# Optimization experiments

Hardware: AMD Instinct MI355X
Metric: run time of the kernel (lower is better)

The kernel has to match this reference:

```python
import jax, jax.numpy as jnp
import numpy as np

L = 4096   # num_tokens (one prefill sequence)
D = 2048   # hidden_size
HK = 16    # num_k_heads
HV = 32    # num_v_heads
DK = 128   # head_k_dim
DV = 128   # head_v_dim
RATIO = HV // HK
EPS = 1e-6


def setup_inputs() -> dict:
    key = jax.random.key(0)
    ks = jax.random.split(key, 11)
    s = 0.02
    return {
        "hidden_states": jax.random.normal(ks[0], (L, D), jnp.float32),
        "Wq": jax.random.normal(ks[1], (D, HK * DK), jnp.float32) * s,
        "Wk": jax.random.normal(ks[2], (D, HK * DK), jnp.float32) * s,
        "Wv": jax.random.normal(ks[3], (D, HV * DV), jnp.float32) * s,
        "Wz": jax.random.normal(ks[4], (D, HV * DV), jnp.float32) * s,
        "Wb": jax.random.normal(ks[5], (D, HV), jnp.float32) * s,
        "Wa": jax.random.normal(ks[6], (D, HV), jnp.float32) * s,
        "A_log": jnp.log(jax.random.uniform(ks[7], (HV,), jnp.float32, 1.0, 16.0)),
        "dt_bias": jax.random.normal(ks[8], (HV,), jnp.float32) * 0.5,
        "norm_weight": jnp.ones((DV,), jnp.float32),
        "W_out": jax.random.normal(ks[9], (HV * DV, D), jnp.float32) * s,
    }


def _l2norm(x):
    return x * jax.lax.rsqrt(jnp.sum(x * x, axis=-1, keepdims=True) + EPS)


def reference(hidden_states, Wq, Wk, Wv, Wz, Wb, Wa, A_log, dt_bias, norm_weight, W_out):
    h = hidden_states
    # --- input projections (qkvz + ba split) ---
    q = _l2norm((h @ Wq).reshape(L, HK, DK))            # [L, HK, DK]
    k = _l2norm((h @ Wk).reshape(L, HK, DK))
    v = (h @ Wv).reshape(L, HV, DV)                     # [L, HV, DV]
    z = (h @ Wz).reshape(L, HV, DV)                     # gate for RMSNorm
    beta = jax.nn.sigmoid(h @ Wb)                       # [L, HV]
    g = -jnp.exp(A_log) * jax.nn.softplus(h @ Wa + dt_bias)  # [L, HV]
    decay = jnp.exp(g)                                  # per-token per-head decay
    # repeat shared q/k heads to value heads (GQA ratio)
    q = jnp.repeat(q, RATIO, axis=1) * (DK ** -0.5)     # [L, HV, DK]
    k = jnp.repeat(k, RATIO, axis=1)

    # --- gated delta rule recurrence over tokens ---
    def step(S, xs):
        q_t, k_t, v_t, b_t, d_t = xs                    # [HV,DK],[HV,DK],[HV,DV],[HV],[HV]
        S = S * d_t[:, None, None]                      # decay state [HV, DK, DV]
        pred = jnp.einsum('hk,hkv->hv', k_t, S)         # memory readout
        delta = (v_t - pred) * b_t[:, None]             # delta-rule correction
        S = S + k_t[:, :, None] * delta[:, None, :]
        o = jnp.einsum('hk,hkv->hv', q_t, S)
        return S, o

    S0 = jnp.zeros((HV, DK, DV), jnp.float32)
    _, core = jax.lax.scan(step, S0, (q, k, v, beta, decay))  # core: [L, HV, DV]

    # --- gated RMSNorm: x * silu(z), rms-normalize over head dim ---
    x = core * jax.nn.silu(z)
    x = x * jax.lax.rsqrt(jnp.mean(x * x, axis=-1, keepdims=True) + EPS) * norm_weight

    # --- output projection ---
    return x.reshape(L, HV * DV) @ W_out                # [L, D]
```

## Files before the change

kernel.cpp:

```cpp
#include <hip/hip_runtime.h>

#define LTOK 4096
#define DHID 2048
#define HKN  16
#define HVN  32
#define DKK  128
#define NTOT 12288

typedef unsigned short u16;
typedef __attribute__((ext_vector_type(8))) short short8;
typedef __attribute__((ext_vector_type(8))) unsigned short u16x8;
typedef __attribute__((ext_vector_type(4))) unsigned short u16x4;
typedef __attribute__((ext_vector_type(4))) float f32x4;

__device__ __forceinline__ float b2f(u16 u) {
  unsigned int x = ((unsigned int)u) << 16;
  return __builtin_bit_cast(float, x);
}
__device__ __forceinline__ u16 f2bf(float f) {
  unsigned int u = __builtin_bit_cast(unsigned int, f);
  u += 0x7FFFu + ((u >> 16) & 1u);
  return (u16)(u >> 16);
}

template<int C> __device__ __forceinline__ float dppmv(float x) {
  int i = __builtin_amdgcn_update_dpp(0, __builtin_bit_cast(int, x), C, 0xF, 0xF, true);
  return __builtin_bit_cast(float, i);
}
__device__ __forceinline__ float red16(float x) {
  x += dppmv<0xB1>(x);
  x += dppmv<0x4E>(x);
  x += dppmv<0x124>(x);
  x += dppmv<0x128>(x);
  return x;
}

__device__ __forceinline__ void gld16(const void* g, void* l) {
  __builtin_amdgcn_global_load_lds((const __attribute__((address_space(1))) void*)g,
                                   (__attribute__((address_space(3))) void*)l, 16, 0, 0);
}

__device__ __forceinline__ int sw16(int r, int c, int rowc) { return (r * rowc + c) ^ ((r & 7) << 3); }

__device__ __forceinline__ void cstore(u16* C, size_t i, float v) { C[i] = f2bf(v); }
__device__ __forceinline__ void cstore(float* C, size_t i, float v) { C[i] = v; }

__global__ __launch_bounds__(256)
void k_cvt(const float* __restrict__ s, u16* __restrict__ d, int n) {
  const int i = (blockIdx.x * 256 + threadIdx.x) * 4;
  const float4 v = *(const float4*)(s + i);
  ushort4 o;
  o.x = f2bf(v.x); o.y = f2bf(v.y); o.z = f2bf(v.z); o.w = f2bf(v.w);
  *(ushort4*)(d + i) = o;
}

__global__ __launch_bounds__(256)
void k_tr(const float* __restrict__ src, u16* __restrict__ dst, int R, int C) {
  __shared__ float tl[32][33];
  const int r0 = blockIdx.y * 32, c0 = blockIdx.x * 32;
  const int tr = threadIdx.x >> 3, tc = (threadIdx.x & 7) * 4;
  const float4 v = *(const float4*)(src + (size_t)(r0 + tr) * C + c0 + tc);
  tl[tr][tc] = v.x; tl[tr][tc + 1] = v.y; tl[tr][tc + 2] = v.z; tl[tr][tc + 3] = v.w;
  __syncthreads();
  ushort4 o;
  o.x = f2bf(tl[tc + 0][tr]); o.y = f2bf(tl[tc + 1][tr]);
  o.z = f2bf(tl[tc + 2][tr]); o.w = f2bf(tl[tc + 3][tr]);
  *(ushort4*)(dst + (size_t)(c0 + tr) * R + r0 + tc) = o;
}

#define MFMA16(a, b, c) __builtin_amdgcn_mfma_f32_16x16x32_bf16(a, b, c, 0, 0, 0)

template<typename OutT>
__global__ __launch_bounds__(512, 2)
void k_g256(const u16* __restrict__ A, const u16* __restrict__ Bt, OutT* __restrict__ C,
            int M, int N, int K, int NT) {
  __shared__ u16 Lds[4][16384];
  const int tid = threadIdx.x;
  const int lane = tid & 63, w = tid >> 6;
  const int fr = lane & 15, fq = lane >> 4;
  const int wm = (w >> 2) * 128, wn = (w & 3) * 64;
  const int nkt = K >> 5;
  const size_t sK = (size_t)K;

  const int MT = gridDim.x / NT;
  const int nts = (NT < 16) ? NT : 16;
  const int per_super = MT * nts;
  const int super = blockIdx.x / per_super;
  const int within = blockIdx.x % per_super;
  const int mtg = MT >> 3;
  const int q = within >> 3;
  const int mt = (within & 7) * mtg + (q % mtg);
  const int nt = super * nts + q / mtg;

  const int kslot = ((tid & 3) ^ ((tid >> 3) & 3)) * 8;
  const u16* aS = A + (size_t)(mt * 256 + (tid >> 2)) * sK + kslot;
  const u16* bS = Bt + (size_t)(nt * 256 + (tid >> 2)) * sK + kslot;

  f32x4 acc[8][4] = {};

#define STAGE(kt_) {                                                          \
    const int sk = ((kt_) < nkt) ? (kt_) : (nkt - 1);                         \
    u16* La = &Lds[(kt_) & 3][w * 512];                                       \
    u16* Lb = &Lds[(kt_) & 3][8192 + w * 512];                                \
    gld16(aS + (size_t)sk * 32, La);                                          \
    gld16(aS + 128 * sK + (size_t)sk * 32, La + 4096);                        \
    gld16(bS + (size_t)sk * 32, Lb);                                          \
    gld16(bS + 128 * sK + (size_t)sk * 32, Lb + 4096); }

  STAGE(0)
  STAGE(1)
  STAGE(2)

  const int akey = (fr >> 1) & 3;
  for (int kt = 0; kt < nkt; ++kt) {
    STAGE(kt + 3)
    asm volatile("s_waitcnt vmcnt(12)" ::: "memory");
    __builtin_amdgcn_s_barrier();
    const u16* Lc = Lds[kt & 3];
    short8 af[8], bf[4];
#pragma unroll
    for (int i = 0; i < 8; ++i)
      af[i] = *(const short8*)&Lc[(wm + i * 16 + fr) * 32 + ((fq ^ akey) << 3)];
#pragma unroll
    for (int j = 0; j < 4; ++j)
      bf[j] = *(const short8*)&Lc[8192 + (wn + j * 16 + fr) * 32 + ((fq ^ akey) << 3)];
    asm volatile("s_waitcnt lgkmcnt(0)" ::: "memory");
    __builtin_amdgcn_s_barrier();
    __builtin_amdgcn_s_setprio(1);
#pragma unroll
    for (int i = 0; i < 8; ++i)
#pragma unroll
      for (int j = 0; j < 4; ++j)
        acc[i][j] = MFMA16(af[i], bf[j], acc[i][j]);
    __builtin_amdgcn_s_setprio(0);
  }
#undef STAGE

  const int r0 = mt * 256 + wm + fq * 4;
  const int c0 = nt * 256 + wn + fr;
#pragma unroll
  for (int i = 0; i < 8; ++i)
#pragma unroll
    for (int j = 0; j < 4; ++j)
#pragma unroll
      for (int e = 0; e < 4; ++e)
        cstore(C, (size_t)(r0 + i * 16 + e) * N + c0 + j * 16, acc[i][j][e]);
}

__global__ __launch_bounds__(256)
void k_ba(const float* __restrict__ h, const float* __restrict__ Wb, const float* __restrict__ Wa,
          const float* __restrict__ A_log, const float* __restrict__ dtb,
          float* __restrict__ beta, float* __restrict__ g_out) {
  const int w = threadIdx.x >> 6, lane = threadIdx.x & 63;
  const int t = blockIdx.x * 4 + w;
  const int j = lane & 31;
  const bool isB = lane < 32;
  const float* __restrict__ hr = h + (size_t)t * DHID;
  const float* Wc = isB ? Wb : Wa;
  float acc = 0.f;
  for (int kk = 0; kk < DHID; ++kk) acc = fmaf(hr[kk], Wc[(size_t)kk * HVN + j], acc);
  if (isB) {
    beta[(size_t)t * HVN + j] = 1.f / (1.f + expf(-acc));
  } else {
    float xx = acc + dtb[j];
    float sp = (xx > 20.f) ? xx : log1pf(expf(xx));
    g_out[(size_t)t * HVN + j] = -expf(A_log[j]) * sp;
  }
}

__global__ __launch_bounds__(256)
void k_l2n(u16* __restrict__ qkvz) {
  const int w = threadIdx.x >> 6, lane = threadIdx.x & 63;
  const int r = blockIdx.x * 4 + w;
  const int isK = r >> 16;
  const int rr = r & 65535;
  const int t = rr >> 4, hd = rr & 15;
  u16* p = qkvz + (size_t)t * NTOT + isK * 2048 + hd * DKK + lane * 2;
  float a = b2f(p[0]), b = b2f(p[1]);
  float ss = a * a + b * b;
  ss = red16(ss);
  ss += __shfl_xor(ss, 16);
  ss += __shfl_xor(ss, 32);
  const float sc = rsqrtf(ss + 1e-6f) * (isK ? 1.f : 0.08838834764831845f);
  p[0] = f2bf(a * sc); p[1] = f2bf(b * sc);
}

__global__ __launch_bounds__(256)
void k_r1(const u16* __restrict__ qkvz, const float* __restrict__ beta_g,
          const float* __restrict__ g_g, u16* __restrict__ UM_g, float* __restrict__ cumL_g) {
  const int pair = blockIdx.x;
  const int hv = pair >> 6, n = pair & 63;
  const int hk = hv >> 1;
  const int t0 = n * 64;
  const int tid = threadIdx.x, lane = tid & 63, wv = tid >> 6;
  const int fr = lane & 15, fq = lane >> 4;

  __shared__ __align__(16) u16 Xb[256 * 64];
  __shared__ __align__(16) u16 Dbuf0[64 * 64 * 2];
  __shared__ __align__(16) u16 Dbuf1[64 * 64 * 2];
  __shared__ float Lc[64];
  __shared__ float Bc[64];
  u16* Kl = Dbuf0;

  const int j = tid & 63, h = tid >> 6;
  const u16* kg = qkvz + (size_t)(t0 + j) * NTOT + 2048 + hk * DKK + h * 32;
  const u16* vg = qkvz + (size_t)(t0 + j) * NTOT + 4096 + hv * DKK + h * 32;
  u16x8 kv[4], vv[4];
#pragma unroll
  for (int i = 0; i < 4; ++i) { kv[i] = *(const u16x8*)(kg + i * 8); vv[i] = *(const u16x8*)(vg + i * 8); }
  if (tid < 64) {
    Lc[tid] = g_g[(size_t)(t0 + tid) * HVN + hv];
    Bc[tid] = beta_g[(size_t)(t0 + tid) * HVN + hv];
  }
#pragma unroll
  for (int i = 0; i < 4; ++i) *(u16x8*)&Kl[sw16(j, h * 32 + i * 8, 128)] = kv[i];
  __syncthreads();
  if (tid == 0) { float a = 0.f; for (int t = 0; t < 64; ++t) { a += Lc[t]; Lc[t] = a; } }
  __syncthreads();
  if (tid < 64) cumL_g[(size_t)pair * 64 + tid] = Lc[tid];

  {
    const float bj = Bc[j];
    const float mj = bj * __expf(Lc[j]);
#pragma unroll
    for (int i = 0; i < 4; ++i)
#pragma unroll
      for (int e = 0; e < 8; ++e) {
        int c = h * 32 + i * 8 + e;
        Xb[sw16(c, j, 64)] = f2bf(bj * b2f(vv[i][e]));
        Xb[sw16(128 + c, j, 64)] = f2bf(mj * b2f(kv[i][e]));
      }
  }
  f32x4 kk[4] = {};
#pragma unroll
  for (int ks = 0; ks < 4; ++ks) {
    short8 afr = *(const short8*)&Kl[sw16(wv * 16 + fr, ks * 32 + fq * 8, 128)];
#pragma unroll
    for (int ct = 0; ct < 4; ++ct) {
      short8 bfr = *(const short8*)&Kl[sw16(ct * 16 + fr, ks * 32 + fq * 8, 128)];
      kk[ct] = MFMA16(afr, bfr, kk[ct]);
    }
  }
  __syncthreads();

  f32x4 acc[16];
#pragma unroll
  for (int ct = 0; ct < 16; ++ct) {
    u16x4 xi = *(const u16x4*)&Xb[sw16(ct * 16 + fr, wv * 16 + fq * 4, 64)];
    acc[ct][0] = b2f(xi[0]); acc[ct][1] = b2f(xi[1]); acc[ct][2] = b2f(xi[2]); acc[ct][3] = b2f(xi[3]);
  }
#pragma unroll
  for (int ct = 0; ct < 4; ++ct) {
    const int s = ct * 16 + fr;
    u16x4 pk;
#pragma unroll
    for (int e = 0; e < 4; ++e) {
      const int t = wv * 16 + fq * 4 + e;
      float v = (s < t) ? -Bc[t] * __expf(Lc[t] - Lc[s]) * kk[ct][e] : 0.f;
      pk[e] = f2bf(v);
      Dbuf0[sw16(t, s, 64)] = pk[e];
    }
    *(u16x4*)&Dbuf0[4096 + sw16(s, wv * 16 + fq * 4, 64)] = pk;
  }
  __syncthreads();

  u16* DA = Dbuf0;
  u16* DB = Dbuf1;
  for (int stg = 0; stg < 6; ++stg) {
    u16* Dr = DA;
    u16* Dc = DA + 4096;
    short8 da0 = *(const short8*)&Dr[sw16(wv * 16 + fr, 0 + fq * 8, 64)];
    short8 da1 = *(const short8*)&Dr[sw16(wv * 16 + fr, 32 + fq * 8, 64)];
#pragma unroll
    for (int ct = 0; ct < 16; ++ct) {
      short8 b0 = *(const short8*)&Xb[sw16(ct * 16 + fr, 0 + fq * 8, 64)];
      short8 b1 = *(const short8*)&Xb[sw16(ct * 16 + fr, 32 + fq * 8, 64)];
      acc[ct] = MFMA16(da0, b0, acc[ct]);
      acc[ct] = MFMA16(da1, b1, acc[ct]);
    }
    f32x4 sq[4] = {};
    if (stg < 5) {
#pragma unroll
      for (int ct = 0; ct < 4; ++ct) {
        short8 sb0 = *(const short8*)&Dc[sw16(ct * 16 + fr, 0 + fq * 8, 64)];
        short8 sb1 = *(const short8*)&Dc[sw16(ct * 16 + fr, 32 + fq * 8, 64)];
        sq[ct] = MFMA16(da0, sb0, sq[ct]);
        sq[ct] = MFMA16(da1, sb1, sq[ct]);
      }
    }
    __syncthreads();
#pragma unroll
    for (int ct = 0; ct < 16; ++ct) {
      u16x4 pk;
      pk[0] = f2bf(acc[ct][0]); pk[1] = f2bf(acc[ct][1]); pk[2] = f2bf(acc[ct][2]); pk[3] = f2bf(acc[ct][3]);
      *(u16x4*)&Xb[sw16(ct * 16 + fr, wv * 16 + fq * 4, 64)] = pk;
    }
    if (stg < 5) {
#pragma unroll
      for (int ct = 0; ct < 4; ++ct) {
        u16x4 pk;
        pk[0] = f2bf(sq[ct][0]); pk[1] = f2bf(sq[ct][1]); pk[2] = f2bf(sq[ct][2]); pk[3] = f2bf(sq[ct][3]);
        *(u16x4*)&(DB + 4096)[sw16(ct * 16 + fr, wv * 16 + fq * 4, 64)] = pk;
#pragma unroll
        for (int e = 0; e < 4; ++e) DB[sw16(wv * 16 + fq * 4 + e, ct * 16 + fr, 64)] = pk[e];
      }
    }
    __syncthreads();
    u16* tmp = DA; DA = DB; DB = tmp;
  }

#pragma unroll
  for (int ct = 0; ct < 16; ++ct) {
    const int c = ct * 16 + fr;
#pragma unroll
    for (int e = 0; e < 4; ++e) {
      const int t = wv * 16 + fq * 4 + e;
      float v = acc[ct][e];
      if (ct >= 8) v = -v;
      UM_g[((size_t)pair * 64 + t) * 256 + c] = f2bf(v);
    }
  }
}

__global__ __launch_bounds__(512)
void k_r2(u16* __restrict__ qkvz, const u16* __restrict__ UM_g,
          const float* __restrict__ cumL_g, u16* __restrict__ o1_g) {
  const int hv = blockIdx.x >> 1, cs = blockIdx.x & 1;
  const int hk = hv >> 1;
  const int tid = threadIdx.x, lane = tid & 63, w = tid >> 6;
  const int fr = lane & 15, fq = lane >> 4;
  const int j = tid & 63, h = tid >> 6;

  __shared__ __align__(16) u16 Ml2[2][8192];
  __shared__ __align__(16) u16 Ql2[2][8192];
  __shared__ __align__(16) u16 Kt2[2][8192];
  __shared__ __align__(16) u16 Ul2[2][4096];
  __shared__ __align__(16) u16 dT[4096];
  __shared__ __align__(16) u16 SbT[8192];
  __shared__ __align__(16) u16 o1b[4096];
  __shared__ float Lc2[2][64];

  const int tw = w & 3;
  const int d0 = (w >> 2) * 2;

  f32x4 sacc[4];
#pragma unroll
  for (int d = 0; d < 4; ++d) sacc[d] = (f32x4){0.f, 0.f, 0.f, 0.f};
  for (int i = tid; i < 8192; i += 512) SbT[i] = 0;

  u16x8 pQ0, pQ1, pK0, pK1, pM0, pM1, pU0;
  float pL, pL63;

#define PREF(nn) {                                                            \
    const int nc = ((nn) < 64) ? (nn) : 63;                                   \
    const int pr = hv * 64 + nc; const int tt0 = nc * 64;                     \
    const u16* qg = qkvz + (size_t)(tt0 + j) * NTOT + hk * DKK + h * 16;      \
    pQ0 = *(const u16x8*)qg;          pQ1 = *(const u16x8*)(qg + 8);          \
    pK0 = *(const u16x8*)(qg + 2048); pK1 = *(const u16x8*)(qg + 2056);       \
    const u16* mg = UM_g + ((size_t)pr * 64 + j) * 256;                       \
    pM0 = *(const u16x8*)(mg + 128 + h * 16);                                 \
    pM1 = *(const u16x8*)(mg + 136 + h * 16);                                 \
    pU0 = *(const u16x8*)(mg + cs * 64 + h * 8);                              \
    pL = cumL_g[(size_t)pr * 64 + j]; pL63 = cumL_g[(size_t)pr * 64 + 63]; }

#define STW(b) {                                                              \
    *(u16x8*)&Ql2[b][sw16(j, h * 16, 128)] = pQ0;                             \
    *(u16x8*)&Ql2[b][sw16(j, h * 16 + 8, 128)] = pQ1;                         \
    *(u16x8*)&Ml2[b][sw16(j, h * 16, 128)] = pM0;                             \
    *(u16x8*)&Ml2[b][sw16(j, h * 16 + 8, 128)] = pM1;                         \
    const float scK = __expf(pL63 - pL);                                      \
    _Pragma("unroll")                                                         \
    for (int e = 0; e < 8; ++e) {                                             \
      Kt2[b][sw16(h * 16 + e, j, 64)] = f2bf(scK * b2f(pK0[e]));              \
      Kt2[b][sw16(h * 16 + 8 + e, j, 64)] = f2bf(scK * b2f(pK1[e]));          \
      Ul2[b][sw16(h * 8 + e, j, 64)] = pU0[e];                                \
    }                                                                         \
    if (h == 0) Lc2[b][j] = pL; }

  PREF(0)
  STW(0)
  __syncthreads();

  for (int n = 0; n < 64; ++n) {
    const int cur = n & 1;
    const int pair = hv * 64 + n, t0 = n * 64;
    const float curL63 = pL63;
    PREF(n + 1)

    short8 amf[4], aqf[4];
#pragma unroll
    for (int ks = 0; ks < 4; ++ks) {
      amf[ks] = *(const short8*)&Ml2[cur][sw16(tw * 16 + fr, ks * 32 + fq * 8, 128)];
      aqf[ks] = *(const short8*)&Ql2[cur][sw16(tw * 16 + fr, ks * 32 + fq * 8, 128)];
    }
    float el[4];
#pragma unroll
    for (int e = 0; e < 4; ++e) el[e] = __expf(Lc2[cur][tw * 16 + fq * 4 + e]);
#pragma unroll
    for (int dd = 0; dd < 2; ++dd) {
      const int d = d0 + dd;
      u16x4 uv = *(const u16x4*)&Ul2[cur][sw16(d * 16 + fr, tw * 16 + fq * 4, 64)];
      f32x4 dc;
      dc[0] = b2f(uv[0]); dc[1] = b2f(uv[1]); dc[2] = b2f(uv[2]); dc[3] = b2f(uv[3]);
      f32x4 oc = {};
#pragma unroll
      for (int ks = 0; ks < 4; ++ks) {
        short8 bs = *(const short8*)&SbT[sw16(d * 16 + fr, ks * 32 + fq * 8, 128)];
        dc = MFMA16(amf[ks], bs, dc);
        oc = MFMA16(aqf[ks], bs, oc);
      }
      u16x4 pk;
      pk[0] = f2bf(dc[0]); pk[1] = f2bf(dc[1]); pk[2] = f2bf(dc[2]); pk[3] = f2bf(dc[3]);
      *(u16x4*)&dT[sw16(d * 16 + fr, tw * 16 + fq * 4, 64)] = pk;
#pragma unroll
      for (int e = 0; e < 4; ++e)
        o1b[sw16(tw * 16 + fq * 4 + e, d * 16 + fr, 64)] = f2bf(oc[e] * el[e]);
    }
    __syncthreads();

    {
      const int i = tid * 8;
      u16x8 vd = *(const u16x8*)&dT[i];
      const int f = cs * 4096 + i;
      *(u16x8*)(qkvz + (size_t)(t0 + (f >> 7)) * NTOT + 4096 + hv * DKK + (f & 127)) = vd;
      u16x8 vo = *(const u16x8*)&o1b[i];
      *(u16x8*)(o1_g + (size_t)pair * 8192 + (size_t)(i >> 6) * 128 + cs * 64 + (i & 63)) = vo;
    }
    STW(cur ^ 1)
    {
      const float eC = __expf(curL63);
      short8 ak0 = *(const short8*)&Kt2[cur][sw16(w * 16 + fr, fq * 8, 64)];
      short8 ak1 = *(const short8*)&Kt2[cur][sw16(w * 16 + fr, 32 + fq * 8, 64)];
#pragma unroll
      for (int d = 0; d < 4; ++d) {
        short8 bd0 = *(const short8*)&dT[sw16(d * 16 + fr, fq * 8, 64)];
        short8 bd1 = *(const short8*)&dT[sw16(d * 16 + fr, 32 + fq * 8, 64)];
        f32x4 sa = sacc[d];
#pragma unroll
        for (int e = 0; e < 4; ++e) sa[e] *= eC;
        sa = MFMA16(ak0, bd0, sa);
        sa = MFMA16(ak1, bd1, sa);
        sacc[d] = sa;
        u16x4 pk;
        pk[0] = f2bf(sa[0]); pk[1] = f2bf(sa[1]); pk[2] = f2bf(sa[2]); pk[3] = f2bf(sa[3]);
        *(u16x4*)&SbT[sw16(d * 16 + fr, w * 16 + fq * 4, 128)] = pk;
      }
    }
    __syncthreads();
  }
#undef PREF
#undef STW
}

__global__ __launch_bounds__(512)
void k_r3(const u16* __restrict__ qkvz, const u16* __restrict__ o1_g,
          const float* __restrict__ cumL_g, const float* __restrict__ nw,
          u16* __restrict__ x) {
  const int pair = blockIdx.x, hv = pair >> 6, n = pair & 63, hk = hv >> 1, t0 = n * 64;
  const int tid = threadIdx.x, lane = tid & 63, w = tid >> 6;
  const int fr = lane & 15, fq = lane >> 4;
  const int j = tid & 63, h = tid >> 6;

  __shared__ __align__(16) u16 Ql[8192];
  __shared__ __align__(16) u16 Kl[8192];
  __shared__ __align__(16) u16 Gl[4096];
  __shared__ __align__(16) u16 dTl[8192];
  __shared__ __align__(16) float of[64 * 132];
  __shared__ float Lc[64];
  __shared__ float Lw[128];

  {
    const u16* qg = qkvz + (size_t)(t0 + j) * NTOT + hk * DKK + h * 16;
    u16x8 q0 = *(const u16x8*)qg, q1 = *(const u16x8*)(qg + 8);
    u16x8 k0 = *(const u16x8*)(qg + 2048), k1 = *(const u16x8*)(qg + 2056);
    *(u16x8*)&Ql[sw16(j, h * 16, 128)] = q0;
    *(u16x8*)&Ql[sw16(j, h * 16 + 8, 128)] = q1;
    *(u16x8*)&Kl[sw16(j, h * 16, 128)] = k0;
    *(u16x8*)&Kl[sw16(j, h * 16 + 8, 128)] = k1;
  }
#pragma unroll
  for (int it = 0; it < 2; ++it) {
    const int f = ((w * 2 + it) * 64 + lane) * 8;
    gld16(qkvz + (size_t)(t0 + (f >> 7)) * NTOT + 4096 + hv * DKK + (f & 127),
          (char*)dTl + (w * 2 + it) * 1024);
  }
  if (tid < 64) Lc[tid] = cumL_g[(size_t)pair * 64 + tid];
  if (tid < 128) Lw[tid] = nw[tid];
  __syncthreads();

  const int tw = w & 3, sp = (w >> 2) * 2;
  {
    f32x4 kk0 = {}, kk1 = {};
#pragma unroll
    for (int ks = 0; ks < 4; ++ks) {
      short8 aq = *(const short8*)&Ql[sw16(tw * 16 + fr, ks * 32 + fq * 8, 128)];
      short8 b0 = *(const short8*)&Kl[sw16(sp * 16 + fr, ks * 32 + fq * 8, 128)];
      short8 b1 = *(const short8*)&Kl[sw16((sp + 1) * 16 + fr, ks * 32 + fq * 8, 128)];
      kk0 = MFMA16(aq, b0, kk0);
      kk1 = MFMA16(aq, b1, kk1);
    }
#pragma unroll
    for (int e = 0; e < 4; ++e) {
      const int t = tw * 16 + fq * 4 + e;
      const float Lt = Lc[t];
      const int s0 = sp * 16 + fr, s1 = s0 + 16;
      Gl[sw16(t, s0, 64)] = f2bf((s0 <= t) ? kk0[e] * __expf(Lt - Lc[s0]) : 0.f);
      Gl[sw16(t, s1, 64)] = f2bf((s1 <= t) ? kk1[e] * __expf(Lt - Lc[s1]) : 0.f);
    }
  }
  __syncthreads();

  {
    short8 ag0 = *(const short8*)&Gl[sw16(tw * 16 + fr, fq * 8, 64)];
    short8 ag1 = *(const short8*)&Gl[sw16(tw * 16 + fr, 32 + fq * 8, 64)];
#pragma unroll
    for (int dd = 0; dd < 4; ++dd) {
      const int d = (w >> 2) * 4 + dd;
      short8 bd0 = *(const short8*)&dTl[sw16(d * 16 + fr, fq * 8, 64)];
      short8 bd1 = *(const short8*)&dTl[sw16(d * 16 + fr, 32 + fq * 8, 64)];
      f32x4 oc = {};
      oc = MFMA16(ag0, bd0, oc);
      oc = MFMA16(ag1, bd1, oc);
#pragma unroll
      for (int e = 0; e < 4; ++e) of[(tw * 16 + fq * 4 + e) * 132 + d * 16 + fr] = oc[e];
    }
  }
  __syncthreads();

  {
    const int t = tid >> 3, q8 = tid & 7;
    const u16* zp = qkvz + (size_t)(t0 + t) * NTOT + 8192 + hv * DKK + q8 * 16;
    const u16* op = o1_g + (size_t)pair * 8192 + t * 128;
    float xv[16];
    float ss = 0.f;
#pragma unroll
    for (int i = 0; i < 2; ++i) {
      u16x8 zv = *(const u16x8*)(zp + i * 8);
      u16x8 ov = *(const u16x8*)(op + (((q8 * 16 + i * 8) ^ ((t & 7) << 3))));
#pragma unroll
      for (int e = 0; e < 8; ++e) {
        float z = b2f(zv[e]);
        float o = of[t * 132 + q8 * 16 + i * 8 + e] + b2f(ov[e]);
        float xx = o * (z / (1.f + __expf(-z)));
        xv[i * 8 + e] = xx;
        ss = fmaf(xx, xx, ss);
      }
    }
    ss += __shfl_xor(ss, 1);
    ss += __shfl_xor(ss, 2);
    ss += __shfl_xor(ss, 4);
    const float scl = rsqrtf(ss * (1.f / 128.f) + 1e-6f);
    u16* xo = x + (size_t)(t0 + t) * 4096 + hv * DKK + q8 * 16;
#pragma unroll
    for (int i = 0; i < 2; ++i) {
      u16x8 pk;
#pragma unroll
      for (int e = 0; e < 8; ++e) pk[e] = f2bf(xv[i * 8 + e] * scl * Lw[q8 * 16 + i * 8 + e]);
      *(u16x8*)(xo + i * 8) = pk;
    }
  }
}

extern "C" void kernel_launch(void* const* d_in, const int* in_sizes, int n_in,
                              void* d_out, int out_size, void* d_ws, size_t ws_size,
                              hipStream_t stream) {
  const float* h    = (const float*)d_in[0];
  const float* Wq   = (const float*)d_in[1];
  const float* Wk   = (const float*)d_in[2];
  const float* Wv   = (const float*)d_in[3];
  const float* Wz   = (const float*)d_in[4];
  const float* Wb   = (const float*)d_in[5];
  const float* Wa   = (const float*)d_in[6];
  const float* Alog = (const float*)d_in[7];
  const float* dtb  = (const float*)d_in[8];
  const float* nw   = (const float*)d_in[9];
  const float* Wo   = (const float*)d_in[10];
  char* ws = (char*)d_ws;
  u16* h_bf  = (u16*)(ws);
  u16* Wt    = (u16*)(ws + 16777216ull);
  u16* UM    = (u16*)(ws);
  u16* Wto   = (u16*)(ws + 67108864ull);
  u16* qkvz  = (u16*)(ws + 83886080ull);
  u16* o1g   = (u16*)(ws + 184549376ull);
  u16* xbuf  = (u16*)(ws + 16777216ull);
  float* beta  = (float*)(ws + 218103808ull);
  float* g     = (float*)(ws + 218103808ull + 524288ull);
  float* cumL  = (float*)(ws + 218103808ull + 1048576ull);

  k_cvt<<<8192, 256, 0, stream>>>(h, h_bf, LTOK * DHID);
  k_tr<<<dim3(64, 64), 256, 0, stream>>>(Wq, Wt, 2048, 2048);
  k_tr<<<dim3(64, 64), 256, 0, stream>>>(Wk, Wt + 2048ull * 2048, 2048, 2048);
  k_tr<<<dim3(128, 64), 256, 0, stream>>>(Wv, Wt + 4096ull * 2048, 2048, 4096);
  k_tr<<<dim3(128, 64), 256, 0, stream>>>(Wz, Wt + 8192ull * 2048, 2048, 4096);
  k_tr<<<dim3(64, 128), 256, 0, stream>>>(Wo, Wto, 4096, 2048);
  k_g256<u16><<<768, 512, 0, stream>>>(h_bf, Wt, qkvz, 4096, 12288, 2048, 48);
  k_ba<<<1024, 256, 0, stream>>>(h, Wb, Wa, Alog, dtb, beta, g);
  k_l2n<<<32768, 256, 0, stream>>>(qkvz);
  k_r1<<<2048, 256, 0, stream>>>(qkvz, beta, g, UM, cumL);
  k_r2<<<64, 512, 0, stream>>>(qkvz, UM, cumL, o1g);
  k_r3<<<2048, 512, 0, stream>>>(qkvz, o1g, cumL, nw, xbuf);
  k_g256<float><<<128, 512, 0, stream>>>(xbuf, Wto, (float*)d_out, 4096, 2048, 4096, 8);
}
```

Measured before the change: 879.5 us.

## Rework GEMM main loop with single barrier, staged LDS reads, narrower output tile

```diff
diff --git a/kernel.cpp b/kernel.cpp
--- a/kernel.cpp
+++ b/kernel.cpp
@@ -38,6 +38,12 @@
 __device__ __forceinline__ void gld16(const void* g, void* l) {
   __builtin_amdgcn_global_load_lds((const __attribute__((address_space(1))) void*)g,
                                    (__attribute__((address_space(3))) void*)l, 16, 0, 0);
+}
+
+template<int OFF> __device__ __forceinline__ short8 dsr(unsigned a) {
+  short8 r;
+  asm volatile("ds_read_b128 %0, %1 offset:%2" : "=v"(r) : "v"(a), "n"(OFF));
+  return r;
 }
 
 __device__ __forceinline__ int sw16(int r, int c, int rowc) { return (r * rowc + c) ^ ((r & 7) << 3); }
@@ -70,15 +76,17 @@
 
 #define MFMA16(a, b, c) __builtin_amdgcn_mfma_f32_16x16x32_bf16(a, b, c, 0, 0, 0)
 
-template<typename OutT>
+template<typename OutT, int NWN>
 __global__ __launch_bounds__(512, 2)
 void k_g256(const u16* __restrict__ A, const u16* __restrict__ Bt, OutT* __restrict__ C,
             int M, int N, int K, int NT) {
-  __shared__ u16 Lds[4][16384];
+  constexpr int BUFE = 8192 + NWN * 2048;
+  constexpr int BN = NWN * 64;
+  __shared__ u16 Lds[4 * BUFE];
   const int tid = threadIdx.x;
   const int lane = tid & 63, w = tid >> 6;
   const int fr = lane & 15, fq = lane >> 4;
-  const int wm = (w >> 2) * 128, wn = (w & 3) * 64;
+  const int wm = (w >> 2) * 128, wn = (w & 3) * (NWN * 16);
   const int nkt = K >> 5;
   const size_t sK = (size_t)K;
 
@@ -94,54 +102,72 @@
 
   const int kslot = ((tid & 3) ^ ((tid >> 3) & 3)) * 8;
   const u16* aS = A + (size_t)(mt * 256 + (tid >> 2)) * sK + kslot;
-  const u16* bS = Bt + (size_t)(nt * 256 + (tid >> 2)) * sK + kslot;
-
-  f32x4 acc[8][4] = {};
-
-#define STAGE(kt_) {                                                          \
-    const int sk = ((kt_) < nkt) ? (kt_) : (nkt - 1);                         \
-    u16* La = &Lds[(kt_) & 3][w * 512];                                       \
-    u16* Lb = &Lds[(kt_) & 3][8192 + w * 512];                                \
-    gld16(aS + (size_t)sk * 32, La);                                          \
-    gld16(aS + 128 * sK + (size_t)sk * 32, La + 4096);                        \
-    gld16(bS + (size_t)sk * 32, Lb);                                          \
-    gld16(bS + 128 * sK + (size_t)sk * 32, Lb + 4096); }
-
-  STAGE(0)
-  STAGE(1)
-  STAGE(2)
+  const u16* bS = Bt + (size_t)(nt * BN + (tid >> 2)) * sK + kslot;
+
+  f32x4 acc[8][NWN] = {};
+
+  auto STAGE = [&](int kt_) {
+    const int sk = (kt_ < nkt) ? kt_ : nkt - 1;
+    u16* base = &Lds[(kt_ & 3) * BUFE];
+    gld16(aS + (size_t)sk * 32, base + w * 512);
+    gld16(aS + 128 * sK + (size_t)sk * 32, base + w * 512 + 4096);
+    gld16(bS + (size_t)sk * 32, base + 8192 + w * 512);
+    if constexpr (NWN == 4)
+      gld16(bS + 128 * sK + (size_t)sk * 32, base + 8192 + w * 512 + 4096);
+  };
+
+  STAGE(0); STAGE(1); STAGE(2);
 
   const int akey = (fr >> 1) & 3;
+  const unsigned ldsBase = (unsigned)(size_t)(__attribute__((address_space(3))) void*)&Lds[0];
+  const unsigned aA0 = ldsBase + 2u * (unsigned)((wm + fr) * 32 + ((fq ^ akey) << 3));
+  const unsigned bA0 = ldsBase + 2u * (unsigned)(8192 + (wn + fr) * 32 + ((fq ^ akey) << 3));
+
   for (int kt = 0; kt < nkt; ++kt) {
-    STAGE(kt + 3)
-    asm volatile("s_waitcnt vmcnt(12)" ::: "memory");
+    if constexpr (NWN == 4) asm volatile("s_waitcnt vmcnt(8)" ::: "memory");
+    else                    asm volatile("s_waitcnt vmcnt(6)" ::: "memory");
     __builtin_amdgcn_s_barrier();
-    const u16* Lc = Lds[kt & 3];
-    short8 af[8], bf[4];
-#pragma unroll
-    for (int i = 0; i < 8; ++i)
-      af[i] = *(const short8*)&Lc[(wm + i * 16 + fr) * 32 + ((fq ^ akey) << 3)];
-#pragma unroll
-    for (int j = 0; j < 4; ++j)
-      bf[j] = *(const short8*)&Lc[8192 + (wn + j * 16 + fr) * 32 + ((fq ^ akey) << 3)];
+    __builtin_amdgcn_sched_barrier(0);
+    STAGE(kt + 3);
+    const unsigned bo = (unsigned)((kt & 3) * BUFE * 2);
+    const unsigned aA = aA0 + bo, bA = bA0 + bo;
+    short8 af[8], bf[NWN];
+    bf[0] = dsr<0>(bA); bf[1] = dsr<1024>(bA);
+    if constexpr (NWN == 4) { bf[2] = dsr<2048>(bA); bf[3] = dsr<3072>(bA); }
+    af[0] = dsr<0>(aA);    af[1] = dsr<1024>(aA);
+    af[2] = dsr<2048>(aA); af[3] = dsr<3072>(aA);
+    af[4] = dsr<4096>(aA); af[5] = dsr<5120>(aA);
+    af[6] = dsr<6144>(aA); af[7] = dsr<7168>(aA);
+    asm volatile("s_waitcnt lgkmcnt(6)" ::: "memory");
+    __builtin_amdgcn_sched_barrier(0);
+    __builtin_amdgcn_s_setprio(1);
+#pragma unroll
+    for (int j = 0; j < NWN; ++j) { acc[0][j] = MFMA16(af[0], bf[j], acc[0][j]);
+                                    acc[1][j] = MFMA16(af[1], bf[j], acc[1][j]); }
+    asm volatile("s_waitcnt lgkmcnt(4)" ::: "memory");
+    __builtin_amdgcn_sched_barrier(0);
+#pragma unroll
+    for (int j = 0; j < NWN; ++j) { acc[2][j] = MFMA16(af[2], bf[j], acc[2][j]);
+                                    acc[3][j] = MFMA16(af[3], bf[j], acc[3][j]); }
+    asm volatile("s_waitcnt lgkmcnt(2)" ::: "memory");
+    __builtin_amdgcn_sched_barrier(0);
+#pragma unroll
+    for (int j = 0; j < NWN; ++j) { acc[4][j] = MFMA16(af[4], bf[j], acc[4][j]);
+                                    acc[5][j] = MFMA16(af[5], bf[j], acc[5][j]); }
     asm volatile("s_waitcnt lgkmcnt(0)" ::: "memory");
-    __builtin_amdgcn_s_barrier();
-    __builtin_amdgcn_s_setprio(1);
-#pragma unroll
-    for (int i = 0; i < 8; ++i)
-#pragma unroll
-      for (int j = 0; j < 4; ++j)
-        acc[i][j] = MFMA16(af[i], bf[j], acc[i][j]);
+    __builtin_amdgcn_sched_barrier(0);
+#pragma unroll
+    for (int j = 0; j < NWN; ++j) { acc[6][j] = MFMA16(af[6], bf[j], acc[6][j]);
+                                    acc[7][j] = MFMA16(af[7], bf[j], acc[7][j]); }
     __builtin_amdgcn_s_setprio(0);
   }
-#undef STAGE
 
   const int r0 = mt * 256 + wm + fq * 4;
-  const int c0 = nt * 256 + wn + fr;
+  const int c0 = nt * BN + wn + fr;
 #pragma unroll
   for (int i = 0; i < 8; ++i)
 #pragma unroll
-    for (int j = 0; j < 4; ++j)
+    for (int j = 0; j < NWN; ++j)
 #pragma unroll
       for (int e = 0; e < 4; ++e)
         cstore(C, (size_t)(r0 + i * 16 + e) * N + c0 + j * 16, acc[i][j][e]);
@@ -593,11 +619,11 @@
   k_tr<<<dim3(128, 64), 256, 0, stream>>>(Wv, Wt + 4096ull * 2048, 2048, 4096);
   k_tr<<<dim3(128, 64), 256, 0, stream>>>(Wz, Wt + 8192ull * 2048, 2048, 4096);
   k_tr<<<dim3(64, 128), 256, 0, stream>>>(Wo, Wto, 4096, 2048);
-  k_g256<u16><<<768, 512, 0, stream>>>(h_bf, Wt, qkvz, 4096, 12288, 2048, 48);
+  k_g256<u16, 4><<<768, 512, 0, stream>>>(h_bf, Wt, qkvz, 4096, 12288, 2048, 48);
   k_ba<<<1024, 256, 0, stream>>>(h, Wb, Wa, Alog, dtb, beta, g);
   k_l2n<<<32768, 256, 0, stream>>>(qkvz);
   k_r1<<<2048, 256, 0, stream>>>(qkvz, beta, g, UM, cumL);
   k_r2<<<64, 512, 0, stream>>>(qkvz, UM, cumL, o1g);
   k_r3<<<2048, 512, 0, stream>>>(qkvz, o1g, cumL, nw, xbuf);
-  k_g256<float><<<128, 512, 0, stream>>>(xbuf, Wto, (float*)d_out, 4096, 2048, 4096, 8);
-}
+  k_g256<float, 2><<<256, 512, 0, stream>>>(xbuf, Wto, (float*)d_out, 4096, 2048, 4096, 16);
+}
```

Result: faster. 831.3 us (-5.5%).
